# Performance work log

Hardware: AMD Instinct MI355X
Metric: run time of the kernel (lower is better)

The kernel has to match this reference:

```python
import jax, jax.numpy as jnp
import numpy as np

TOP_K_FRACTION = 0.1


def setup_inputs() -> dict:
    key = jax.random.key(0)
    k1, k2, k3 = jax.random.split(key, 3)
    B, H, S, D = 2, 12, 1024, 64
    q = jax.random.normal(k1, (B, H, S, D), dtype=jnp.float32)
    k = jax.random.normal(k2, (B, H, S, D), dtype=jnp.float32)
    v = jax.random.normal(k3, (B, H, S, D), dtype=jnp.float32)
    mask = jnp.zeros((B, 1, 1, S), dtype=jnp.float32)
    return {"q": q, "k": k, "v": v, "mask": mask}


def reference(q, k, v, mask):
    B, H, S, D = q.shape
    k_precise = max(1, int(S * TOP_K_FRACTION))
    # binary (sign) approximation of attention scores; detached like torch
    q_bin = jnp.sign(jax.lax.stop_gradient(q))
    k_bin = jnp.sign(jax.lax.stop_gradient(k))
    approx_scores = jnp.einsum('bhsd,bhtd->bhst', q_bin, k_bin) / D  # [B,H,S,S]
    _, topk_idx = jax.lax.top_k(approx_scores, k_precise)  # [B,H,S,kp]
    # gather top-k keys/values per query: [B,H,S,kp,D]
    k_gathered = jnp.take_along_axis(k[:, :, None, :, :], topk_idx[..., None], axis=3)
    v_gathered = jnp.take_along_axis(v[:, :, None, :, :], topk_idx[..., None], axis=3)
    scale = np.float32(1.0 / np.sqrt(D))
    precise_scores = jnp.einsum('bhsd,bhskd->bhsk', q, k_gathered) * scale
    # gather mask along key positions: mask [B,1,1,S] -> [B,H,S,kp]
    mask_gathered = jnp.take_along_axis(
        jnp.broadcast_to(mask, (B, H, S, S)), topk_idx, axis=-1)
    precise_scores = precise_scores + mask_gathered
    precise_probs = jax.nn.softmax(precise_scores, axis=-1)
    attn_output = jnp.einsum('bhsk,bhskd->bhsd', precise_probs, v_gathered)
    return attn_output
```

## Files before the change

kernel.cpp:

```cpp
#include <hip/hip_runtime.h>
#include <hip/hip_fp16.h>
#include <cstdint>

#define BB 2
#define HH 12
#define SS 1024
#define DD 64
#define KP 102
#define QPB 4

typedef _Float16 half2v __attribute__((ext_vector_type(2)));
typedef _Float16 half8v __attribute__((ext_vector_type(8)));
typedef float    f32x4  __attribute__((ext_vector_type(4)));

__device__ __forceinline__ int mbcnt64(unsigned long long m) {
    return (int)__builtin_amdgcn_mbcnt_hi((unsigned)(m >> 32),
               __builtin_amdgcn_mbcnt_lo((unsigned)(m & 0xffffffffull), 0u));
}

__device__ __forceinline__ void gl_lds16(const void* g, void* l) {
    __builtin_amdgcn_global_load_lds(
        (const __attribute__((address_space(1))) unsigned int*)g,
        (__attribute__((address_space(3))) unsigned int*)l,
        16, 0, 0);
}

__global__ __launch_bounds__(256) void prep_kernel(
    const float* __restrict__ k, const float* __restrict__ v,
    unsigned long long* __restrict__ kbits, _Float16* __restrict__ kh,
    _Float16* __restrict__ vT)
{
    const int t = (int)threadIdx.x, w = t >> 6, lane = t & 63;
    const int kb64 = (int)blockIdx.x * 64;
    const int bh = kb64 >> 10, keybase = kb64 & (SS - 1);

    #pragma unroll
    for (int e = 0; e < 16; ++e) {
        int row = kb64 + w * 16 + e;
        float kv = k[(size_t)row * DD + lane];
        unsigned long long km = __ballot(kv > 0.0f);
        kh[(size_t)row * DD + lane] = (_Float16)(kv * 0.125f);
        if (lane == 0) kbits[row] = km;
    }

    __shared__ _Float16 lds[64][66];
    #pragma unroll
    for (int e = 0; e < 16; ++e) {
        int key = e * 4 + w;
        int dim = t & 63;
        lds[key][dim] = (_Float16)v[((size_t)kb64 + key) * DD + dim];
    }
    __syncthreads();
    #pragma unroll
    for (int e = 0; e < 16; ++e) {
        int dim = e * 4 + w;
        int key = t & 63;
        vT[((size_t)bh * DD + dim) * SS + keybase + key] = lds[key][dim];
    }
}

__global__ __launch_bounds__(256, 4) void select_kernel(
    const float* __restrict__ q,
    const unsigned long long* __restrict__ kbits,
    unsigned long long* __restrict__ selmask)
{
    const int tid  = (int)threadIdx.x;
    const int w    = tid >> 6;
    const int lane = tid & 63;
    const int query = (int)blockIdx.x * QPB + w;
    const int bh    = query >> 10;

    const float qreg = q[(size_t)query * DD + lane];
    const unsigned long long qm = __ballot(qreg > 0.0f);

    const unsigned long long* kb = kbits + (size_t)bh * SS;
    int pbin[16];
    #pragma unroll
    for (int j = 0; j < 16; ++j)
        pbin[j] = (int)__popcll(qm ^ kb[j * 64 + lane]);

    #define COUNT_LE(P, OUTC)                                      \
        { int _c = 0;                                              \
          _Pragma("unroll")                                        \
          for (int j = 0; j < 16; ++j)                             \
              _c += (int)__popcll(__ballot(pbin[j] <= (P)));       \
          (OUTC) = _c; }
    int P = 27, c, clt;
    COUNT_LE(P, c);
    if (c >= KP) {
        COUNT_LE(P - 1, clt);
        while (clt >= KP) { c = clt; --P; COUNT_LE(P - 1, clt); }
    } else {
        do { clt = c; ++P; COUNT_LE(P, c); } while (c < KP);
    }
    const int binP = P;
    const int need = KP - clt;
    #undef COUNT_LE

    unsigned long long* selq = selmask + (size_t)query * 16;
    int tie_base = 0;
    #pragma unroll
    for (int j = 0; j < 16; ++j) {
        bool isGt  = pbin[j] < binP;
        bool isTie = (pbin[j] == binP);
        unsigned long long tiem = __ballot(isTie);
        int rank = tie_base + mbcnt64(tiem);
        bool take = isGt || (isTie && rank < need);
        unsigned long long tm = __ballot(take);
        if (lane == 0) selq[j] = tm;
        tie_base += (int)__popcll(tiem);
    }
}

__global__ __launch_bounds__(128, 4) void attn_kernel(
    const float* __restrict__ q, const _Float16* __restrict__ kh,
    const _Float16* __restrict__ vT, const float* __restrict__ mask,
    const unsigned long long* __restrict__ selmask,
    float* __restrict__ out)
{
    const int tid  = (int)threadIdx.x;
    const int wq   = tid >> 6;
    const int lane = tid & 63;
    const int r    = lane & 15;
    const int g    = lane >> 4;
    const int qbase = (int)blockIdx.x * 32;
    const int bh = qbase >> 10;
    const int b  = bh / HH;
    const int query = qbase + wq * 16 + r;
    const int g4 = g * 4;

    __shared__ char sK[8192];
    __shared__ char sV[8192];
    __shared__ char sP[2][2048];

    half8v qf[2];
    #pragma unroll
    for (int ks = 0; ks < 2; ++ks) {
        const float* qp = q + (size_t)query * DD + ks * 32 + g * 8;
        float4 f0 = *(const float4*)qp;
        float4 f1 = *(const float4*)(qp + 4);
        half8v h;
        h[0] = (_Float16)f0.x; h[1] = (_Float16)f0.y;
        h[2] = (_Float16)f0.z; h[3] = (_Float16)f0.w;
        h[4] = (_Float16)f1.x; h[5] = (_Float16)f1.y;
        h[6] = (_Float16)f1.z; h[7] = (_Float16)f1.w;
        qf[ks] = h;
    }

    const char* khb = (const char*)(kh + (size_t)bh * SS * DD);
    const char* vTb = (const char*)(vT + (size_t)bh * DD * SS);
    const float* maskb = mask + (size_t)b * SS;
    const unsigned long long* selq = selmask + (size_t)query * 16;
    char* sPw = sP[wq];

    f32x4 oacc[4];
    #pragma unroll
    for (int db = 0; db < 4; ++db) oacc[db] = (f32x4){0.f, 0.f, 0.f, 0.f};
    float l_part = 0.0f;

    #pragma unroll 1
    for (int kt = 0; kt < 16; ++kt) {
        #pragma unroll
        for (int i = 0; i < 4; ++i) {
            const int c   = i * 128 + tid;
            const int row = c >> 3, ch = c & 7;
            const int sch = ch ^ (row & 7);
            const void* gK = khb + (((size_t)(kt * 64 + row)) << 7) + (sch << 4);
            const void* gV = vTb + (((size_t)row) << 11) + ((size_t)kt << 7) + (sch << 4);
            char* lK = sK + ((i * 128 + wq * 64) << 4);
            char* lV = sV + ((i * 128 + wq * 64) << 4);
            gl_lds16(gK, lK);
            gl_lds16(gV, lV);
        }
        const unsigned long long smkt = selq[kt];
        __syncthreads();

        f32x4 ct[4];
        #pragma unroll
        for (int mt = 0; mt < 4; ++mt) {
            const int row = mt * 16 + r;
            half8v ka0 = *(const half8v*)&sK[(row << 7) + ((( g    ) ^ (r & 7)) << 4)];
            half8v ka1 = *(const half8v*)&sK[(row << 7) + (((4 + g) ^ (r & 7)) << 4)];
            f32x4 cc = (f32x4){0.f, 0.f, 0.f, 0.f};
            cc = __builtin_amdgcn_mfma_f32_16x16x32_f16(ka0, qf[0], cc, 0, 0, 0);
            cc = __builtin_amdgcn_mfma_f32_16x16x32_f16(ka1, qf[1], cc, 0, 0, 0);
            ct[mt] = cc;
        }

        #pragma unroll
        for (int mt = 0; mt < 4; ++mt) {
            float4 mv = *(const float4*)(maskb + kt * 64 + mt * 16 + g4);
            const unsigned sw = (unsigned)(smkt >> (mt * 16));
            float mvj[4] = {mv.x, mv.y, mv.z, mv.w};
            float e[4];
            #pragma unroll
            for (int j = 0; j < 4; ++j) {
                float s  = ct[mt][j] + mvj[j];
                float ev = __expf(s);
                ev = ((sw >> (g4 + j)) & 1u) ? ev : 0.0f;
                e[j] = ev;
                l_part += ev;
            }
            half2v p0; p0[0] = (_Float16)e[0]; p0[1] = (_Float16)e[1];
            half2v p1; p1[0] = (_Float16)e[2]; p1[1] = (_Float16)e[3];
            char* wp = sPw + (r << 7) + ((((mt * 2) + (g >> 1)) ^ (r & 7)) << 4)
                           + ((g & 1) << 3);
            ((half2v*)wp)[0] = p0;
            ((half2v*)wp)[1] = p1;
        }

        #pragma unroll
        for (int ks = 0; ks < 2; ++ks) {
            half8v pf = *(const half8v*)&sPw[(r << 7) + (((ks * 4 + g) ^ (r & 7)) << 4)];
            #pragma unroll
            for (int db = 0; db < 4; ++db) {
                const int vrow = db * 16 + r;
                half8v va = *(const half8v*)&sV[(vrow << 7) + (((ks * 4 + g) ^ (r & 7)) << 4)];
                oacc[db] = __builtin_amdgcn_mfma_f32_16x16x32_f16(va, pf, oacc[db], 0, 0, 0);
            }
        }
        __syncthreads();
    }

    l_part += __shfl_xor(l_part, 16);
    l_part += __shfl_xor(l_part, 32);
    const float rinv = __frcp_rn(l_part);
    #pragma unroll
    for (int db = 0; db < 4; ++db) {
        float4 o = make_float4(oacc[db][0] * rinv, oacc[db][1] * rinv,
                               oacc[db][2] * rinv, oacc[db][3] * rinv);
        *(float4*)(out + (size_t)query * DD + db * 16 + g4) = o;
    }
}

extern "C" void kernel_launch(void* const* d_in, const int* in_sizes, int n_in,
                              void* d_out, int out_size, void* d_ws, size_t ws_size,
                              hipStream_t stream) {
    const float* q    = (const float*)d_in[0];
    const float* k    = (const float*)d_in[1];
    const float* v    = (const float*)d_in[2];
    const float* mask = (const float*)d_in[3];
    float* out = (float*)d_out;

    const int rows = BB * HH * SS;
    char* ws = (char*)d_ws;
    unsigned long long* kbits = (unsigned long long*)ws;
    _Float16* kh = (_Float16*)(ws + (size_t)rows * 8);
    _Float16* vT = (_Float16*)(ws + (size_t)rows * 8
                                  + (size_t)rows * DD * 2);
    unsigned long long* selmask = (unsigned long long*)(ws + (size_t)rows * 8
                                  + 2 * (size_t)rows * DD * 2);

    prep_kernel<<<rows / 64, 256, 0, stream>>>(k, v, kbits, kh, vT);
    select_kernel<<<rows / QPB, 256, 0, stream>>>(q, kbits, selmask);
    attn_kernel<<<rows / 32, 128, 0, stream>>>(q, kh, vT, mask, selmask, out);
}
```

Measured before the change: 122.1 us.

## Double-buffer K/V LDS tiles to overlap global loads with MFMA compute

Splits the K/V tile path into a stage step and a compute step and ping-pongs between two LDS buffers. The next tile's async global-to-LDS loads are issued before the current tile's QK, softmax and PV work, so memory latency can hide behind compute instead of stalling at each barrier. The cost is double the K/V LDS footprint per block, which could limit occupancy, and a manually unrolled two-tile loop.

After: 125.5 us. +2.7%, slower.

```diff
diff --git a/kernel.cpp b/kernel.cpp
--- a/kernel.cpp
+++ b/kernel.cpp
@@ -129,8 +129,8 @@
     const int query = qbase + wq * 16 + r;
     const int g4 = g * 4;
 
-    __shared__ char sK[8192];
-    __shared__ char sV[8192];
+    __shared__ char sK0[8192], sV0[8192];
+    __shared__ char sK1[8192], sV1[8192];
     __shared__ char sP[2][2048];
 
     half8v qf[2];
@@ -158,8 +158,7 @@
     for (int db = 0; db < 4; ++db) oacc[db] = (f32x4){0.f, 0.f, 0.f, 0.f};
     float l_part = 0.0f;
 
-    #pragma unroll 1
-    for (int kt = 0; kt < 16; ++kt) {
+    auto stage = [&](char* sKb, char* sVb, int kt) {
         #pragma unroll
         for (int i = 0; i < 4; ++i) {
             const int c   = i * 128 + tid;
@@ -167,26 +166,25 @@
             const int sch = ch ^ (row & 7);
             const void* gK = khb + (((size_t)(kt * 64 + row)) << 7) + (sch << 4);
             const void* gV = vTb + (((size_t)row) << 11) + ((size_t)kt << 7) + (sch << 4);
-            char* lK = sK + ((i * 128 + wq * 64) << 4);
-            char* lV = sV + ((i * 128 + wq * 64) << 4);
-            gl_lds16(gK, lK);
-            gl_lds16(gV, lV);
-        }
+            gl_lds16(gK, sKb + ((i * 128 + wq * 64) << 4));
+            gl_lds16(gV, sVb + ((i * 128 + wq * 64) << 4));
+        }
+        __builtin_amdgcn_sched_barrier(0);
+    };
+
+    auto compute = [&](const char* sKb, const char* sVb, int kt) {
         const unsigned long long smkt = selq[kt];
-        __syncthreads();
-
         f32x4 ct[4];
         #pragma unroll
         for (int mt = 0; mt < 4; ++mt) {
             const int row = mt * 16 + r;
-            half8v ka0 = *(const half8v*)&sK[(row << 7) + ((( g    ) ^ (r & 7)) << 4)];
-            half8v ka1 = *(const half8v*)&sK[(row << 7) + (((4 + g) ^ (r & 7)) << 4)];
+            half8v ka0 = *(const half8v*)&sKb[(row << 7) + ((( g    ) ^ (r & 7)) << 4)];
+            half8v ka1 = *(const half8v*)&sKb[(row << 7) + (((4 + g) ^ (r & 7)) << 4)];
             f32x4 cc = (f32x4){0.f, 0.f, 0.f, 0.f};
             cc = __builtin_amdgcn_mfma_f32_16x16x32_f16(ka0, qf[0], cc, 0, 0, 0);
             cc = __builtin_amdgcn_mfma_f32_16x16x32_f16(ka1, qf[1], cc, 0, 0, 0);
             ct[mt] = cc;
         }
-
         #pragma unroll
         for (int mt = 0; mt < 4; ++mt) {
             float4 mv = *(const float4*)(maskb + kt * 64 + mt * 16 + g4);
@@ -208,17 +206,28 @@
             ((half2v*)wp)[0] = p0;
             ((half2v*)wp)[1] = p1;
         }
-
         #pragma unroll
         for (int ks = 0; ks < 2; ++ks) {
             half8v pf = *(const half8v*)&sPw[(r << 7) + (((ks * 4 + g) ^ (r & 7)) << 4)];
             #pragma unroll
             for (int db = 0; db < 4; ++db) {
                 const int vrow = db * 16 + r;
-                half8v va = *(const half8v*)&sV[(vrow << 7) + (((ks * 4 + g) ^ (r & 7)) << 4)];
+                half8v va = *(const half8v*)&sVb[(vrow << 7) + (((ks * 4 + g) ^ (r & 7)) << 4)];
                 oacc[db] = __builtin_amdgcn_mfma_f32_16x16x32_f16(va, pf, oacc[db], 0, 0, 0);
             }
         }
+    };
+
+    stage(sK0, sV0, 0);
+    __syncthreads();
+    #pragma unroll 1
+    for (int kt2 = 0; kt2 < 8; ++kt2) {
+        const int kt = kt2 * 2;
+        stage(sK1, sV1, kt + 1);
+        compute(sK0, sV0, kt);
+        __syncthreads();
+        if (kt2 < 7) stage(sK0, sV0, kt + 2);
+        compute(sK1, sV1, kt + 1);
         __syncthreads();
     }
 
```
